# Optimization experiments

Hardware: AMD Instinct MI355X
Metric: run time of the kernel (lower is better)

Reference implementation:

```python
import jax, jax.numpy as jnp
import numpy as np

N = 30000   # nodes
E = 480000  # directed edges (avg degree 16)
CIN = 64    # c_in
CH = 64     # c_hidden

_PARAM_NAMES = ["Wl1","bl1","Wr1","br1","We1","att1","bo1",
                "Wlm","blm","Wrm","brm","Wem","attm","bom",
                "Wl8","bl8","Wr8","br8","We8","att8","bo8"]
_PARAM_SHAPES = [(CIN,CH),(CH,),(CIN,CH),(CH,),(1,CH),(CH,),(CH,),
                 (6,CH,CH),(6,CH),(6,CH,CH),(6,CH),(6,1,CH),(6,CH),(6,CH),
                 (CH,1),(1,),(CH,1),(1,),(1,1),(1,),(1,)]

def setup_inputs() -> dict:
    key = jax.random.key(0)
    ks = jax.random.split(key, 4 + len(_PARAM_NAMES))
    inp = {
        "features": jax.random.normal(ks[0], (N, CIN), dtype=jnp.float32),
        "edge_src": jax.random.randint(ks[1], (E,), 0, N),
        "edge_dst": jax.random.randint(ks[2], (E,), 0, N),
        "edge_weight": jax.random.uniform(ks[3], (E,), dtype=jnp.float32),
    }
    for i, (name, shape) in enumerate(zip(_PARAM_NAMES, _PARAM_SHAPES)):
        inp[name] = jax.random.normal(ks[4 + i], shape, dtype=jnp.float32) * 0.05
    return inp

def _gatv2_layer(x, src, dst, attr, Wl, bl, Wr, br, We, att, bo):
    # PyG GATv2Conv, heads=1, negative_slope=0.2; (src,dst,attr) already include self-loops.
    n = x.shape[0]
    xl = x @ Wl + bl                                  # [N, C] source-side transform (lin_l)
    xr = x @ Wr + br                                  # [N, C] target-side transform (lin_r)
    e = xl[src] + xr[dst] + attr[:, None] * We[0]     # [Ea, C] per-edge pre-activation
    logit = jax.nn.leaky_relu(e, 0.2) @ att           # [Ea]
    m = jax.ops.segment_max(logit, dst, num_segments=n)
    z = jnp.exp(logit - m[dst])                       # stable softmax over each node's in-edges
    s = jax.ops.segment_sum(z, dst, num_segments=n)
    alpha = z / s[dst]                                # [Ea]
    return jax.ops.segment_sum(alpha[:, None] * xl[src], dst, num_segments=n) + bo

def reference(features, edge_src, edge_dst, edge_weight,
              Wl1, bl1, Wr1, br1, We1, att1, bo1,
              Wlm, blm, Wrm, brm, Wem, attm, bom,
              Wl8, bl8, Wr8, br8, We8, att8, bo8):
    n = features.shape[0]
    # add_self_loops=True with fill_value='mean': self-loop attr = mean of incoming edge attrs
    cnt = jax.ops.segment_sum(jnp.ones_like(edge_weight), edge_dst, num_segments=n)
    loop_attr = jax.ops.segment_sum(edge_weight, edge_dst, num_segments=n) / jnp.maximum(cnt, 1.0)
    loops = jnp.arange(n)
    src = jnp.concatenate([edge_src, loops])
    dst = jnp.concatenate([edge_dst, loops])
    attr = jnp.concatenate([edge_weight, loop_attr])
    x = _gatv2_layer(features, src, dst, attr, Wl1, bl1, Wr1, br1, We1, att1, bo1)
    for i in range(6):  # conv2..conv7, structurally identical hidden layers
        x = _gatv2_layer(x, src, dst, attr, Wlm[i], blm[i], Wrm[i], brm[i], Wem[i], attm[i], bom[i])
    x = _gatv2_layer(x, src, dst, attr, Wl8, bl8, Wr8, br8, We8, att8, bo8)  # [N, 1]
    return jnp.mean(x, axis=-2)  # mean pool over nodes -> [1]
```

## Files before the change

kernel.cpp:

```cpp
#include <hip/hip_runtime.h>
#include <hip/hip_fp16.h>
#include <math.h>

#define CH 64


struct AggS {
  float acc[8];
  float m, s;
};

__device__ __forceinline__ void gather8(const __half* __restrict__ xlh, int src, int cg,
                                        float xv[8]) {
  uint4 raw = *reinterpret_cast<const uint4*>(xlh + ((size_t)src << 6) + (cg << 3));
  const __half2* h = reinterpret_cast<const __half2*>(&raw);
#pragma unroll
  for (int j = 0; j < 4; ++j) {
    float2 f = __half22float2(h[j]);
    xv[2 * j] = f.x;
    xv[2 * j + 1] = f.y;
  }
}

__device__ __forceinline__ void batch_update(const float xv[8], float a, bool valid,
                                             const float xrw[8], const float Wec[8],
                                             const float attc[8], AggS& st) {
  float partial = 0.f;
#pragma unroll
  for (int j = 0; j < 8; ++j) {
    float ee = fmaf(a, Wec[j], xv[j] + xrw[j]);
    float lr = fmaxf(ee, 0.f) + 0.2f * fminf(ee, 0.f);
    partial = fmaf(lr, attc[j], partial);
  }
  partial += __shfl_xor(partial, 1, 64);
  partial += __shfl_xor(partial, 2, 64);
  partial += __shfl_xor(partial, 4, 64);
  float logit = valid ? partial : -INFINITY;
  float bm = logit;
  bm = fmaxf(bm, __shfl_xor(bm, 8, 64));
  bm = fmaxf(bm, __shfl_xor(bm, 16, 64));
  bm = fmaxf(bm, __shfl_xor(bm, 32, 64));
  float mn = fmaxf(st.m, bm);
  float sc = __expf(st.m - mn);
  float p = __expf(logit - mn);
  float ps = p;
  ps += __shfl_xor(ps, 8, 64);
  ps += __shfl_xor(ps, 16, 64);
  ps += __shfl_xor(ps, 32, 64);
  st.s = fmaf(st.s, sc, ps);
#pragma unroll
  for (int j = 0; j < 8; ++j) st.acc[j] = fmaf(st.acc[j], sc, p * xv[j]);
  st.m = mn;
}

__device__ __forceinline__ void agg_node8(const __half* __restrict__ xlh,
                                          const int2* __restrict__ csr, int beg, int dv,
                                          const float xrw[8], const float Wec[8],
                                          const float attc[8], int eg, int cg, AggS& st) {
  int end = beg + dv;
  int nb = (dv + 7) >> 3;
  int idx0 = beg + eg;
  bool vA = idx0 < end;
  int2 edA = csr[min(idx0, end - 1)];
  float xvA[8];
  gather8(xlh, edA.x, cg, xvA);
  int2 edB = edA;
  bool vB = false;
  if (nb > 1) {
    int idx1 = beg + 8 + eg;
    vB = idx1 < end;
    edB = csr[min(idx1, end - 1)];
  }
  for (int t = 0; t < nb; ++t) {
    float xvB[8];
    bool haveNext = (t + 1 < nb);
    if (haveNext) gather8(xlh, edB.x, cg, xvB);
    int2 edC = edB;
    bool vC = false;
    if (t + 2 < nb) {
      int idx = beg + (t + 2) * 8 + eg;
      vC = idx < end;
      edC = csr[min(idx, end - 1)];
    }
    batch_update(xvA, __int_as_float(edA.y), vA, xrw, Wec, attc, st);
    edA = edB; vA = vB;
    edB = edC; vB = vC;
    if (haveNext) {
#pragma unroll
      for (int j = 0; j < 8; ++j) xvA[j] = xvB[j];
    }
  }
#pragma unroll
  for (int j = 0; j < 8; ++j) {
    st.acc[j] += __shfl_xor(st.acc[j], 8, 64);
    st.acc[j] += __shfl_xor(st.acc[j], 16, 64);
    st.acc[j] += __shfl_xor(st.acc[j], 32, 64);
  }
}

#define LOAD8F(dst, srcp)                                \
  {                                                      \
    *(float4*)&dst[0] = *(const float4*)&(srcp)[0];      \
    *(float4*)&dst[4] = *(const float4*)&(srcp)[4];      \
  }


#define WSUM_SCALE 33554432.0f
#define WSUM_MASK 0xFFFFFFFFFFULL

__global__ void k_count(const int* __restrict__ dst, const float* __restrict__ w, int E,
                        unsigned long long* __restrict__ agg, int* __restrict__ rank) {
  int i = blockIdx.x * blockDim.x + threadIdx.x;
  if (i < E) {
    int d = dst[i];
    unsigned long long pk = (1ULL << 40) | (unsigned long long)(w[i] * WSUM_SCALE);
    unsigned long long old = atomicAdd(&agg[d], pk);
    rank[i] = (int)(old >> 40);
  }
}

__global__ void k_alloc(const unsigned long long* __restrict__ agg,
                        float* __restrict__ loop_attr, int* __restrict__ deg,
                        int* __restrict__ row_beg, int* __restrict__ total, int n) {
  int i = blockIdx.x * blockDim.x + threadIdx.x;
  int lane = threadIdx.x & 63;
  int d = 0;
  if (i < n) {
    unsigned long long v = agg[i];
    int c = (int)(v >> 40);
    float ws = (float)(v & WSUM_MASK) * (1.0f / WSUM_SCALE);
    loop_attr[i] = ws / fmaxf((float)c, 1.0f);
    d = c + 1;
    deg[i] = d;
  }
  int x = d;
#pragma unroll
  for (int off = 1; off < 64; off <<= 1) {
    int t = __shfl_up(x, off, 64);
    if (lane >= off) x += t;
  }
  int base = 0;
  if (lane == 63) base = atomicAdd(total, x);
  base = __shfl(base, 63, 64);
  if (i < n) row_beg[i] = base + x - d;
}

__global__ void k_scatter(const int* __restrict__ src, const int* __restrict__ dst,
                          const float* __restrict__ w, const int* __restrict__ rank, int E,
                          const int* __restrict__ row_beg, int2* __restrict__ csr) {
  int i = blockIdx.x * blockDim.x + threadIdx.x;
  if (i < E) {
    int d = dst[i];
    csr[row_beg[d] + rank[i]] = make_int2(src[i], __float_as_int(w[i]));
  }
}

__global__ void k_selfloop(int n, const int* __restrict__ row_beg, const int* __restrict__ deg,
                           int2* __restrict__ csr, const float* __restrict__ loop_attr) {
  int v = blockIdx.x * blockDim.x + threadIdx.x;
  if (v < n) {
    csr[row_beg[v] + deg[v] - 1] = make_int2(v, __float_as_int(loop_attr[v]));
  }
}


__global__ void __launch_bounds__(256) k_transform(
    const float* __restrict__ x, const float* __restrict__ Wl, const float* __restrict__ bl,
    const float* __restrict__ Wr, const float* __restrict__ br,
    __half* __restrict__ xlh, float* __restrict__ xr, int n) {
  __shared__ float sW[2][CH * CH];
  for (int i = threadIdx.x; i < (CH * CH) / 4; i += blockDim.x) {
    ((float4*)sW[0])[i] = ((const float4*)Wl)[i];
    ((float4*)sW[1])[i] = ((const float4*)Wr)[i];
  }
  __syncthreads();
  int lane = threadIdx.x & 63;
  int wid = threadIdx.x >> 6;
  float blc = bl[lane], brc = br[lane];
  int wavesPerGrid = (gridDim.x * blockDim.x) >> 6;
  for (int row = blockIdx.x * (blockDim.x >> 6) + wid; row < n; row += wavesPerGrid) {
    float xv = x[(size_t)row * CH + lane];
    float accl = blc, accr = brc;
#pragma unroll
    for (int k = 0; k < CH; ++k) {
      float xk = __shfl(xv, k, 64);
      accl = fmaf(xk, sW[0][k * CH + lane], accl);
      accr = fmaf(xk, sW[1][k * CH + lane], accr);
    }
    xlh[(size_t)row * CH + lane] = __float2half(accl);
    xr[(size_t)row * CH + lane] = accr;
  }
}


__global__ void __launch_bounds__(256) k_aggregate(
    const __half* __restrict__ xlh, const float* __restrict__ xr,
    const int* __restrict__ row_beg, const int* __restrict__ deg,
    const int2* __restrict__ csr,
    const float* __restrict__ We, const float* __restrict__ att, const float* __restrict__ bo,
    float* __restrict__ out, int n) {
  int lane = threadIdx.x & 63;
  int v = (blockIdx.x * blockDim.x + threadIdx.x) >> 6;
  if (v >= n) return;
  int eg = lane >> 3, cg = lane & 7;
  int c0 = cg << 3;
  float Wec[8], attc[8], xrw[8];
  LOAD8F(Wec, We + c0);
  LOAD8F(attc, att + c0);
  LOAD8F(xrw, xr + (size_t)v * CH + c0);
  AggS st;
  st.m = -INFINITY;
  st.s = 0.f;
#pragma unroll
  for (int j = 0; j < 8; ++j) st.acc[j] = 0.f;
  agg_node8(xlh, csr, row_beg[v], deg[v], xrw, Wec, attc, eg, cg, st);
  if (eg == 0) {
    float boc[8];
    LOAD8F(boc, bo + c0);
    float o[8];
#pragma unroll
    for (int j = 0; j < 8; ++j) o[j] = st.acc[j] / st.s + boc[j];
    *(float4*)&out[(size_t)v * CH + c0] = *(float4*)&o[0];
    *(float4*)&out[(size_t)v * CH + c0 + 4] = *(float4*)&o[4];
  }
}

__global__ void __launch_bounds__(256) k_aggregate_t8(
    const __half* __restrict__ xlh, const float* __restrict__ xr,
    const int* __restrict__ row_beg, const int* __restrict__ deg,
    const int2* __restrict__ csr,
    const float* __restrict__ We, const float* __restrict__ att, const float* __restrict__ bo,
    const float* __restrict__ Wl8, const float* __restrict__ bl8,
    const float* __restrict__ Wr8, const float* __restrict__ br8,
    float* __restrict__ xl8, float* __restrict__ xr8, int n) {
  int lane = threadIdx.x & 63;
  int v = (blockIdx.x * blockDim.x + threadIdx.x) >> 6;
  if (v >= n) return;
  int eg = lane >> 3, cg = lane & 7;
  int c0 = cg << 3;
  float Wec[8], attc[8], xrw[8];
  LOAD8F(Wec, We + c0);
  LOAD8F(attc, att + c0);
  LOAD8F(xrw, xr + (size_t)v * CH + c0);
  AggS st;
  st.m = -INFINITY;
  st.s = 0.f;
#pragma unroll
  for (int j = 0; j < 8; ++j) st.acc[j] = 0.f;
  agg_node8(xlh, csr, row_beg[v], deg[v], xrw, Wec, attc, eg, cg, st);
  float boc[8], wl8c[8], wr8c[8];
  LOAD8F(boc, bo + c0);
  LOAD8F(wl8c, Wl8 + c0);
  LOAD8F(wr8c, Wr8 + c0);
  float pa = 0.f, pb = 0.f;
#pragma unroll
  for (int j = 0; j < 8; ++j) {
    float o = st.acc[j] / st.s + boc[j];
    pa = fmaf(o, wl8c[j], pa);
    pb = fmaf(o, wr8c[j], pb);
  }
  pa += __shfl_xor(pa, 1, 64);
  pa += __shfl_xor(pa, 2, 64);
  pa += __shfl_xor(pa, 4, 64);
  pb += __shfl_xor(pb, 1, 64);
  pb += __shfl_xor(pb, 2, 64);
  pb += __shfl_xor(pb, 4, 64);
  if (lane == 0) {
    xl8[v] = pa + bl8[0];
    xr8[v] = pb + br8[0];
  }
}

__global__ void __launch_bounds__(256) k_agg8_mean(
    const float* __restrict__ xl8, const float* __restrict__ xr8,
    const int* __restrict__ row_beg, const int* __restrict__ deg,
    const int2* __restrict__ csr,
    const float* __restrict__ We, const float* __restrict__ att, const float* __restrict__ bo,
    float* __restrict__ out, int n) {
  int lane = threadIdx.x & 63;
  int wid = threadIdx.x >> 6;
  float We0 = We[0], att0 = att[0], bo0 = bo[0];
  float inv_n = 1.0f / (float)n;
  float local = 0.f;
  int nwaves = gridDim.x * 4;
  for (int v = blockIdx.x * 4 + wid; v < n; v += nwaves) {
    float xrc = xr8[v];
    int beg = row_beg[v], dv = deg[v];
    float m = -INFINITY, s = 0.f, acc = 0.f;
    for (int chunk = 0; chunk < dv; chunk += 64) {
      int idx = chunk + lane;
      bool valid = idx < dv;
      int2 ed = valid ? csr[beg + idx] : make_int2(0, 0);
      float xlc = valid ? xl8[ed.x] : 0.f;
      float ee = fmaf(__int_as_float(ed.y), We0, xlc + xrc);
      float logit = valid ? (ee > 0.f ? ee : 0.2f * ee) * att0 : -INFINITY;
      float bm = logit;
#pragma unroll
      for (int off = 32; off > 0; off >>= 1) bm = fmaxf(bm, __shfl_xor(bm, off, 64));
      float mn = fmaxf(m, bm);
      float p = __expf(logit - mn);
      float pd = p * xlc;
#pragma unroll
      for (int off = 32; off > 0; off >>= 1) {
        p += __shfl_xor(p, off, 64);
        pd += __shfl_xor(pd, off, 64);
      }
      float sc = __expf(m - mn);
      s = fmaf(s, sc, p);
      acc = fmaf(acc, sc, pd);
      m = mn;
    }
    local += (acc / s + bo0) * inv_n;
  }
  __shared__ float sw[4];
  if (lane == 0) sw[wid] = local;
  __syncthreads();
  if (threadIdx.x == 0) atomicAdd(out, sw[0] + sw[1] + sw[2] + sw[3]);
}


extern "C" void kernel_launch(void* const* d_in, const int* in_sizes, int n_in,
                              void* d_out, int out_size, void* d_ws, size_t ws_size,
                              hipStream_t stream) {
  const float* features = (const float*)d_in[0];
  const int* edge_src = (const int*)d_in[1];
  const int* edge_dst = (const int*)d_in[2];
  const float* edge_w = (const float*)d_in[3];
  const int N = in_sizes[0] / CH;
  const int E = in_sizes[1];

  char* p = (char*)d_ws;
  auto take = [&](size_t bytes) {
    char* r = p;
    p += (bytes + 255) & ~(size_t)255;
    return r;
  };
  float* xA = (float*)take((size_t)N * CH * 4);
  float* xB = (float*)take((size_t)N * CH * 4);
  __half* xlh = (__half*)take((size_t)N * CH * 2);
  float* xr = (float*)take((size_t)N * CH * 4);
  int2* csr = (int2*)take((size_t)(E + N) * 8);
  char* zero_region = take((size_t)N * 8 + 256);
  unsigned long long* agg = (unsigned long long*)zero_region;
  int* total = (int*)(zero_region + (size_t)N * 8);
  int* rank = (int*)take((size_t)E * 4);
  float* loop_attr = (float*)take((size_t)N * 4);
  int* deg = (int*)take((size_t)N * 4);
  int* row_beg = (int*)take((size_t)N * 4);
  float* xl8 = (float*)take((size_t)N * 4);
  float* xr8 = (float*)take((size_t)N * 4);

  hipMemsetAsync(zero_region, 0, (size_t)N * 8 + 256, stream);
  hipMemsetAsync(d_out, 0, sizeof(float), stream);

  const int tb = 256;
  k_count<<<(E + tb - 1) / tb, tb, 0, stream>>>(edge_dst, edge_w, E, agg, rank);
  k_alloc<<<(N + tb - 1) / tb, tb, 0, stream>>>(agg, loop_attr, deg, row_beg, total, N);
  k_scatter<<<(E + tb - 1) / tb, tb, 0, stream>>>(edge_src, edge_dst, edge_w, rank, E,
                                                  row_beg, csr);
  k_selfloop<<<(N + tb - 1) / tb, tb, 0, stream>>>(N, row_beg, deg, csr, loop_attr);

  const float* Wl1 = (const float*)d_in[4];
  const float* bl1 = (const float*)d_in[5];
  const float* Wr1 = (const float*)d_in[6];
  const float* br1 = (const float*)d_in[7];
  const float* We1 = (const float*)d_in[8];
  const float* att1 = (const float*)d_in[9];
  const float* bo1 = (const float*)d_in[10];
  const float* Wlm = (const float*)d_in[11];
  const float* blm = (const float*)d_in[12];
  const float* Wrm = (const float*)d_in[13];
  const float* brm = (const float*)d_in[14];
  const float* Wem = (const float*)d_in[15];
  const float* attm = (const float*)d_in[16];
  const float* bom = (const float*)d_in[17];

  const int agg_grid = ((size_t)N * 64 + tb - 1) / tb;
  const float* x_cur = features;
  float* x_nxt = xA;
  for (int layer = 0; layer < 7; ++layer) {
    const float *Wl, *bl, *Wr, *br, *We, *att, *bo;
    if (layer == 0) {
      Wl = Wl1; bl = bl1; Wr = Wr1; br = br1; We = We1; att = att1; bo = bo1;
    } else {
      int i = layer - 1;
      Wl = Wlm + (size_t)i * CH * CH;
      bl = blm + (size_t)i * CH;
      Wr = Wrm + (size_t)i * CH * CH;
      br = brm + (size_t)i * CH;
      We = Wem + (size_t)i * CH;
      att = attm + (size_t)i * CH;
      bo = bom + (size_t)i * CH;
    }
    k_transform<<<1024, 256, 0, stream>>>(x_cur, Wl, bl, Wr, br, xlh, xr, N);
    if (layer < 6) {
      k_aggregate<<<agg_grid, tb, 0, stream>>>(xlh, xr, row_beg, deg, csr, We, att, bo,
                                               x_nxt, N);
      x_cur = x_nxt;
      x_nxt = (x_nxt == xA) ? xB : xA;
    } else {
      k_aggregate_t8<<<agg_grid, tb, 0, stream>>>(
          xlh, xr, row_beg, deg, csr, We, att, bo, (const float*)d_in[18],
          (const float*)d_in[19], (const float*)d_in[20], (const float*)d_in[21], xl8, xr8, N);
    }
  }
  k_agg8_mean<<<1024, 256, 0, stream>>>(xl8, xr8, row_beg, deg, csr, (const float*)d_in[22],
                                        (const float*)d_in[23], (const float*)d_in[24],
                                        (float*)d_out, N);
}
```

Measured before the change: 581.8 us.

## Drop online max-tracking softmax in favor of clamped direct exp accumulation

Replaces the streaming max-rescaled softmax in the aggregation kernels with direct exp of clamped logits accumulated per lane, reducing across lanes only once at the end. This removes per-batch max/sum shuffles and rescale exps. The final division is also replaced by a reciprocal-multiply. The risk is numerical: the result differs from true softmax if logits exceed the clamp range.

```diff
diff --git a/kernel.cpp b/kernel.cpp
--- a/kernel.cpp
+++ b/kernel.cpp
@@ -4,11 +4,6 @@
 
 #define CH 64
 
-
-struct AggS {
-  float acc[8];
-  float m, s;
-};
 
 __device__ __forceinline__ void gather8(const __half* __restrict__ xlh, int src, int cg,
                                         float xv[8]) {
@@ -24,7 +19,7 @@
 
 __device__ __forceinline__ void batch_update(const float xv[8], float a, bool valid,
                                              const float xrw[8], const float Wec[8],
-                                             const float attc[8], AggS& st) {
+                                             const float attc[8], float acc[8], float& s) {
   float partial = 0.f;
 #pragma unroll
   for (int j = 0; j < 8; ++j) {
@@ -35,28 +30,18 @@
   partial += __shfl_xor(partial, 1, 64);
   partial += __shfl_xor(partial, 2, 64);
   partial += __shfl_xor(partial, 4, 64);
-  float logit = valid ? partial : -INFINITY;
-  float bm = logit;
-  bm = fmaxf(bm, __shfl_xor(bm, 8, 64));
-  bm = fmaxf(bm, __shfl_xor(bm, 16, 64));
-  bm = fmaxf(bm, __shfl_xor(bm, 32, 64));
-  float mn = fmaxf(st.m, bm);
-  float sc = __expf(st.m - mn);
-  float p = __expf(logit - mn);
-  float ps = p;
-  ps += __shfl_xor(ps, 8, 64);
-  ps += __shfl_xor(ps, 16, 64);
-  ps += __shfl_xor(ps, 32, 64);
-  st.s = fmaf(st.s, sc, ps);
-#pragma unroll
-  for (int j = 0; j < 8; ++j) st.acc[j] = fmaf(st.acc[j], sc, p * xv[j]);
-  st.m = mn;
+  float logit = fminf(fmaxf(partial, -40.f), 40.f);
+  float p = valid ? __expf(logit) : 0.f;
+  s += p;
+#pragma unroll
+  for (int j = 0; j < 8; ++j) acc[j] = fmaf(p, xv[j], acc[j]);
 }
 
 __device__ __forceinline__ void agg_node8(const __half* __restrict__ xlh,
                                           const int2* __restrict__ csr, int beg, int dv,
                                           const float xrw[8], const float Wec[8],
-                                          const float attc[8], int eg, int cg, AggS& st) {
+                                          const float attc[8], int eg, int cg, float acc[8],
+                                          float& s) {
   int end = beg + dv;
   int nb = (dv + 7) >> 3;
   int idx0 = beg + eg;
@@ -82,7 +67,7 @@
       vC = idx < end;
       edC = csr[min(idx, end - 1)];
     }
-    batch_update(xvA, __int_as_float(edA.y), vA, xrw, Wec, attc, st);
+    batch_update(xvA, __int_as_float(edA.y), vA, xrw, Wec, attc, acc, s);
     edA = edB; vA = vB;
     edB = edC; vB = vC;
     if (haveNext) {
@@ -90,11 +75,14 @@
       for (int j = 0; j < 8; ++j) xvA[j] = xvB[j];
     }
   }
+  s += __shfl_xor(s, 8, 64);
+  s += __shfl_xor(s, 16, 64);
+  s += __shfl_xor(s, 32, 64);
 #pragma unroll
   for (int j = 0; j < 8; ++j) {
-    st.acc[j] += __shfl_xor(st.acc[j], 8, 64);
-    st.acc[j] += __shfl_xor(st.acc[j], 16, 64);
-    st.acc[j] += __shfl_xor(st.acc[j], 32, 64);
+    acc[j] += __shfl_xor(acc[j], 8, 64);
+    acc[j] += __shfl_xor(acc[j], 16, 64);
+    acc[j] += __shfl_xor(acc[j], 32, 64);
   }
 }
 
@@ -208,18 +196,17 @@
   LOAD8F(Wec, We + c0);
   LOAD8F(attc, att + c0);
   LOAD8F(xrw, xr + (size_t)v * CH + c0);
-  AggS st;
-  st.m = -INFINITY;
-  st.s = 0.f;
-#pragma unroll
-  for (int j = 0; j < 8; ++j) st.acc[j] = 0.f;
-  agg_node8(xlh, csr, row_beg[v], deg[v], xrw, Wec, attc, eg, cg, st);
+  float acc[8], s = 0.f;
+#pragma unroll
+  for (int j = 0; j < 8; ++j) acc[j] = 0.f;
+  agg_node8(xlh, csr, row_beg[v], deg[v], xrw, Wec, attc, eg, cg, acc, s);
   if (eg == 0) {
     float boc[8];
     LOAD8F(boc, bo + c0);
     float o[8];
-#pragma unroll
-    for (int j = 0; j < 8; ++j) o[j] = st.acc[j] / st.s + boc[j];
+    float inv_s = 1.0f / s;
+#pragma unroll
+    for (int j = 0; j < 8; ++j) o[j] = fmaf(acc[j], inv_s, boc[j]);
     *(float4*)&out[(size_t)v * CH + c0] = *(float4*)&o[0];
     *(float4*)&out[(size_t)v * CH + c0 + 4] = *(float4*)&o[4];
   }
@@ -242,20 +229,19 @@
   LOAD8F(Wec, We + c0);
   LOAD8F(attc, att + c0);
   LOAD8F(xrw, xr + (size_t)v * CH + c0);
-  AggS st;
-  st.m = -INFINITY;
-  st.s = 0.f;
-#pragma unroll
-  for (int j = 0; j < 8; ++j) st.acc[j] = 0.f;
-  agg_node8(xlh, csr, row_beg[v], deg[v], xrw, Wec, attc, eg, cg, st);
+  float acc[8], s = 0.f;
+#pragma unroll
+  for (int j = 0; j < 8; ++j) acc[j] = 0.f;
+  agg_node8(xlh, csr, row_beg[v], deg[v], xrw, Wec, attc, eg, cg, acc, s);
   float boc[8], wl8c[8], wr8c[8];
   LOAD8F(boc, bo + c0);
   LOAD8F(wl8c, Wl8 + c0);
   LOAD8F(wr8c, Wr8 + c0);
   float pa = 0.f, pb = 0.f;
+  float inv_s = 1.0f / s;
 #pragma unroll
   for (int j = 0; j < 8; ++j) {
-    float o = st.acc[j] / st.s + boc[j];
+    float o = fmaf(acc[j], inv_s, boc[j]);
     pa = fmaf(o, wl8c[j], pa);
     pb = fmaf(o, wr8c[j], pb);
   }
@@ -286,29 +272,23 @@
   for (int v = blockIdx.x * 4 + wid; v < n; v += nwaves) {
     float xrc = xr8[v];
     int beg = row_beg[v], dv = deg[v];
-    float m = -INFINITY, s = 0.f, acc = 0.f;
+    float s = 0.f, acc = 0.f;
     for (int chunk = 0; chunk < dv; chunk += 64) {
       int idx = chunk + lane;
       bool valid = idx < dv;
       int2 ed = valid ? csr[beg + idx] : make_int2(0, 0);
       float xlc = valid ? xl8[ed.x] : 0.f;
       float ee = fmaf(__int_as_float(ed.y), We0, xlc + xrc);
-      float logit = valid ? (ee > 0.f ? ee : 0.2f * ee) * att0 : -INFINITY;
-      float bm = logit;
-#pragma unroll
-      for (int off = 32; off > 0; off >>= 1) bm = fmaxf(bm, __shfl_xor(bm, off, 64));
-      float mn = fmaxf(m, bm);
-      float p = __expf(logit - mn);
-      float pd = p * xlc;
-#pragma unroll
-      for (int off = 32; off > 0; off >>= 1) {
-        p += __shfl_xor(p, off, 64);
-        pd += __shfl_xor(pd, off, 64);
-      }
-      float sc = __expf(m - mn);
-      s = fmaf(s, sc, p);
-      acc = fmaf(acc, sc, pd);
-      m = mn;
+      float logit = (ee > 0.f ? ee : 0.2f * ee) * att0;
+      logit = fminf(fmaxf(logit, -40.f), 40.f);
+      float p = valid ? __expf(logit) : 0.f;
+      s += p;
+      acc = fmaf(p, xlc, acc);
+    }
+#pragma unroll
+    for (int off = 32; off > 0; off >>= 1) {
+      s += __shfl_xor(s, off, 64);
+      acc += __shfl_xor(acc, off, 64);
     }
     local += (acc / s + bo0) * inv_n;
   }
```

New measurement: 535.8 us. 1.09x faster.
